# Kernel optimization log

Hardware: AMD Instinct MI355X
Metric: run time of the kernel (lower is better)

Reference implementation:

```python
import jax, jax.numpy as jnp
from jax import lax
import numpy as np

B, S, HID = 1, 1024, 4096
H, D = 64, 64  # num_heads, head_size (hidden = H*D)


def setup_inputs() -> dict:
    key = jax.random.key(0)
    ks = jax.random.split(key, 14)
    s = 0.02  # weight init scale
    return {
        "hidden": jax.random.normal(ks[0], (B, S, HID), jnp.float32),
        "w_key": jax.random.normal(ks[1], (HID, HID), jnp.float32) * s,
        "w_value": jax.random.normal(ks[2], (HID, HID), jnp.float32) * s,
        "w_receptance": jax.random.normal(ks[3], (HID, HID), jnp.float32) * s,
        "w_gate": jax.random.normal(ks[4], (HID, HID), jnp.float32) * s,
        "w_output": jax.random.normal(ks[5], (HID, HID), jnp.float32) * s,
        "time_mix_key": jax.random.uniform(ks[6], (HID,), jnp.float32),
        "time_mix_value": jax.random.uniform(ks[7], (HID,), jnp.float32),
        "time_mix_receptance": jax.random.uniform(ks[8], (HID,), jnp.float32),
        "time_mix_gate": jax.random.uniform(ks[9], (HID,), jnp.float32),
        "time_decay": jax.random.normal(ks[10], (H, D), jnp.float32) * 0.5,
        "time_faaaa": jax.random.normal(ks[11], (H, D), jnp.float32) * 0.5,
        "gn_weight": jnp.ones((HID,), jnp.float32),
        "gn_bias": jnp.zeros((HID,), jnp.float32),
    }


def reference(hidden, w_key, w_value, w_receptance, w_gate, w_output,
              time_mix_key, time_mix_value, time_mix_receptance, time_mix_gate,
              time_decay, time_faaaa, gn_weight, gn_bias):
    b, s, hid = hidden.shape
    h, d = time_decay.shape

    # time_shift: shifted[t] = hidden[t-1], shifted[0] = 0 (state is None)
    shifted = jnp.concatenate([jnp.zeros_like(hidden[:, :1]), hidden[:, :-1]], axis=1)

    def mix(m):
        return hidden * m + shifted * (1.0 - m)

    k = mix(time_mix_key) @ w_key.T            # (b, s, hid)
    v = mix(time_mix_value) @ w_value.T
    r = mix(time_mix_receptance) @ w_receptance.T
    g = jax.nn.silu(mix(time_mix_gate) @ w_gate.T)

    def heads(x):  # (b, s, hid) -> (s, b, h, d) for scan over time
        return x.reshape(b, s, h, d).transpose(1, 0, 2, 3)

    kh, vh, rh = heads(k), heads(v), heads(r)

    td = jnp.exp(-jnp.exp(time_decay))[None, :, :, None]  # (1, h, d, 1)
    tf = time_faaaa[None, :, :, None]                      # (1, h, d, 1)

    def step(state, rkv):
        r_t, k_t, v_t = rkv                                # each (b, h, d)
        a = k_t[..., :, None] * v_t[..., None, :]          # (b, h, d, d) outer product
        o = jnp.einsum('bhd,bhde->bhe', r_t, tf * a + state)
        return a + td * state, o

    state0 = jnp.zeros((b, h, d, d), jnp.float32)
    _, out = lax.scan(step, state0, (rh, kh, vh))          # out: (s, b, h, d)
    out = out.transpose(1, 0, 2, 3).reshape(b, s, hid)

    # GroupNorm(num_groups=h, channels=hid) over flattened tokens
    x = out.reshape(b * s, h, d)
    mu = x.mean(-1, keepdims=True)
    var = x.var(-1, keepdims=True)
    xn = (x - mu) * lax.rsqrt(var + 1e-5)
    xn = xn.reshape(b * s, hid) * gn_weight + gn_bias
    xn = xn.reshape(b, s, hid)

    return (g * xn) @ w_output.T
```

## Files before the change

kernel.cpp:

```cpp
#include <hip/hip_runtime.h>

#define S_LEN 1024
#define HIDN  4096
#define NH    64
#define HD    64
#define NCH   32
#define CLEN  32

typedef short bf16x8 __attribute__((ext_vector_type(8)));
typedef float f32x4  __attribute__((ext_vector_type(4)));

__device__ __forceinline__ unsigned short f2bf(float x){
  unsigned u = __float_as_uint(x);
  u += 0x7fffu + ((u >> 16) & 1u);
  return (unsigned short)(u >> 16);
}

__device__ __forceinline__ void gload_lds16(const void* g, void* l){
  __builtin_amdgcn_global_load_lds(
      (const __attribute__((address_space(1))) void*)g,
      (__attribute__((address_space(3))) void*)l, 16, 0, 0);
}

__global__ __launch_bounds__(256)
void wconv_kernel(const float* __restrict__ w0, const float* __restrict__ w1,
                  const float* __restrict__ w2, const float* __restrict__ w3,
                  const float* __restrict__ w4, unsigned short* __restrict__ out)
{
  const int z = blockIdx.y;
  const float* __restrict__ w = (z==0)?w0:(z==1)?w1:(z==2)?w2:(z==3)?w3:w4;
  const size_t idx = (size_t)blockIdx.x * 2048 + (size_t)threadIdx.x * 8;
  float4 a = *(const float4*)(w + idx);
  float4 b = *(const float4*)(w + idx + 4);
  ushort4 lo, hi;
  lo.x = f2bf(a.x); lo.y = f2bf(a.y); lo.z = f2bf(a.z); lo.w = f2bf(a.w);
  hi.x = f2bf(b.x); hi.y = f2bf(b.y); hi.z = f2bf(b.z); hi.w = f2bf(b.w);
  unsigned short* o = out + (size_t)z * HIDN * HIDN + idx;
  *(ushort4*)(o)     = lo;
  *(ushort4*)(o + 4) = hi;
}

__global__ __launch_bounds__(256)
void mix_kernel(const float* __restrict__ hidden,
                const float* __restrict__ tmk, const float* __restrict__ tmv,
                const float* __restrict__ tmr, const float* __restrict__ tmg,
                unsigned short* __restrict__ mixed)
{
  int idx = blockIdx.x * 256 + threadIdx.x;
  int i = idx & (HIDN - 1);
  float h  = hidden[idx];
  float sh = (idx >= HIDN) ? hidden[idx - HIDN] : 0.f;
  float mk = tmk[i], mv = tmv[i], mr = tmr[i], mg = tmg[i];
  mixed[idx + 0 * S_LEN * HIDN] = f2bf(h * mk + sh * (1.f - mk));
  mixed[idx + 1 * S_LEN * HIDN] = f2bf(h * mv + sh * (1.f - mv));
  mixed[idx + 2 * S_LEN * HIDN] = f2bf(h * mr + sh * (1.f - mr));
  mixed[idx + 3 * S_LEN * HIDN] = f2bf(h * mg + sh * (1.f - mg));
}

__global__ __launch_bounds__(256)
void gemm_lds(const unsigned short* __restrict__ Aall,
              const unsigned short* __restrict__ Wall,
              float* __restrict__ Call, int silu_mask, int nzper)
{
  const int bid  = blockIdx.x;
  const int xcd  = bid & 7;
  const int slot = bid >> 3;
  const int mt   = slot & 7;
  const int nz   = xcd * nzper + (slot >> 3);
  const int nt   = nz & 31;
  const int z    = nz >> 5;

  const unsigned short* __restrict__ A = Aall + (size_t)z * S_LEN * HIDN;
  const unsigned short* __restrict__ W = Wall + (size_t)z * HIDN * HIDN;
  float* __restrict__ C = Call + (size_t)z * S_LEN * HIDN;
  const int m0 = mt * 128;
  const int n0 = nt * 128;

  __shared__ unsigned short As[2][128 * 32];
  __shared__ unsigned short Bs[2][128 * 32];

  const int tid  = threadIdx.x;
  const int lane = tid & 63;
  const int wave = tid >> 6;
  const int wr = (wave >> 1) * 64;
  const int wc = (wave & 1) * 64;
  const int fr = lane & 15;
  const int fk = (lane >> 4) * 8;

  const int q0 = tid, q1 = 256 + tid;
  const int r0 = q0 >> 2, c0 = (q0 & 3) * 8;
  const int r1 = q1 >> 2, c1 = (q1 & 3) * 8;
  const unsigned short* A0 = A + (size_t)(m0 + r0) * HIDN + c0;
  const unsigned short* A1 = A + (size_t)(m0 + r1) * HIDN + c1;
  const unsigned short* W0 = W + (size_t)(n0 + r0) * HIDN + c0;
  const unsigned short* W1 = W + (size_t)(n0 + r1) * HIDN + c1;

  f32x4 acc[4][4];
#pragma unroll
  for (int mi = 0; mi < 4; ++mi)
#pragma unroll
    for (int ni = 0; ni < 4; ++ni) acc[mi][ni] = (f32x4){0.f, 0.f, 0.f, 0.f};

  for (int k0 = 0; k0 < HIDN; k0 += 64) {
    gload_lds16(A0 + k0,      &As[0][q0 * 8]);
    gload_lds16(A1 + k0,      &As[0][q1 * 8]);
    gload_lds16(A0 + k0 + 32, &As[1][q0 * 8]);
    gload_lds16(A1 + k0 + 32, &As[1][q1 * 8]);
    gload_lds16(W0 + k0,      &Bs[0][q0 * 8]);
    gload_lds16(W1 + k0,      &Bs[0][q1 * 8]);
    gload_lds16(W0 + k0 + 32, &Bs[1][q0 * 8]);
    gload_lds16(W1 + k0 + 32, &Bs[1][q1 * 8]);
    __syncthreads();

#pragma unroll
    for (int kk = 0; kk < 2; ++kk) {
      bf16x8 af[4], bq[4];
#pragma unroll
      for (int mi = 0; mi < 4; ++mi)
        af[mi] = *(const bf16x8*)(&As[kk][(wr + mi * 16 + fr) * 32 + fk]);
#pragma unroll
      for (int ni = 0; ni < 4; ++ni)
        bq[ni] = *(const bf16x8*)(&Bs[kk][(wc + ni * 16 + fr) * 32 + fk]);
#pragma unroll
      for (int mi = 0; mi < 4; ++mi)
#pragma unroll
        for (int ni = 0; ni < 4; ++ni)
          acc[mi][ni] = __builtin_amdgcn_mfma_f32_16x16x32_bf16(af[mi], bq[ni], acc[mi][ni], 0, 0, 0);
    }
    __syncthreads();
  }

  const bool do_silu = (silu_mask >> z) & 1;
  const int orow = (lane >> 4) * 4;
#pragma unroll
  for (int mi = 0; mi < 4; ++mi)
#pragma unroll
    for (int ni = 0; ni < 4; ++ni)
#pragma unroll
      for (int r = 0; r < 4; ++r) {
        int row = m0 + wr + mi * 16 + orow + r;
        int col = n0 + wc + ni * 16 + fr;
        float v = acc[mi][ni][r];
        if (do_silu) v = v / (1.f + __expf(-v));
        C[(size_t)row * HIDN + col] = v;
      }
}

__global__ __launch_bounds__(256)
void gemm_splitk(const unsigned short* __restrict__ A,
                 const unsigned short* __restrict__ W,
                 float* __restrict__ C)
{
  const int bid  = blockIdx.x;
  const int xcd  = bid & 7;
  const int slot = bid >> 3;
  const int mt   = slot & 7;
  const int nl   = (slot >> 3) & 3;
  const int ks   = slot >> 5;
  const int nt   = xcd * 4 + nl;
  const int m0 = mt * 128, n0 = nt * 128;
  const int kb = ks * (HIDN / 2), ke = kb + (HIDN / 2);

  __shared__ unsigned short As[2][128 * 32];
  __shared__ unsigned short Bs[2][128 * 32];

  const int tid  = threadIdx.x;
  const int lane = tid & 63;
  const int wave = tid >> 6;
  const int wr = (wave >> 1) * 64;
  const int wc = (wave & 1) * 64;
  const int fr = lane & 15;
  const int fk = (lane >> 4) * 8;

  const int q0 = tid, q1 = 256 + tid;
  const int r0 = q0 >> 2, c0 = (q0 & 3) * 8;
  const int r1 = q1 >> 2, c1 = (q1 & 3) * 8;
  const unsigned short* A0 = A + (size_t)(m0 + r0) * HIDN + c0;
  const unsigned short* A1 = A + (size_t)(m0 + r1) * HIDN + c1;
  const unsigned short* W0 = W + (size_t)(n0 + r0) * HIDN + c0;
  const unsigned short* W1 = W + (size_t)(n0 + r1) * HIDN + c1;

  f32x4 acc[4][4];
#pragma unroll
  for (int mi = 0; mi < 4; ++mi)
#pragma unroll
    for (int ni = 0; ni < 4; ++ni) acc[mi][ni] = (f32x4){0.f, 0.f, 0.f, 0.f};

  for (int k0 = kb; k0 < ke; k0 += 64) {
    gload_lds16(A0 + k0,      &As[0][q0 * 8]);
    gload_lds16(A1 + k0,      &As[0][q1 * 8]);
    gload_lds16(A0 + k0 + 32, &As[1][q0 * 8]);
    gload_lds16(A1 + k0 + 32, &As[1][q1 * 8]);
    gload_lds16(W0 + k0,      &Bs[0][q0 * 8]);
    gload_lds16(W1 + k0,      &Bs[0][q1 * 8]);
    gload_lds16(W0 + k0 + 32, &Bs[1][q0 * 8]);
    gload_lds16(W1 + k0 + 32, &Bs[1][q1 * 8]);
    __syncthreads();

#pragma unroll
    for (int kk = 0; kk < 2; ++kk) {
      bf16x8 af[4], bq[4];
#pragma unroll
      for (int mi = 0; mi < 4; ++mi)
        af[mi] = *(const bf16x8*)(&As[kk][(wr + mi * 16 + fr) * 32 + fk]);
#pragma unroll
      for (int ni = 0; ni < 4; ++ni)
        bq[ni] = *(const bf16x8*)(&Bs[kk][(wc + ni * 16 + fr) * 32 + fk]);
#pragma unroll
      for (int mi = 0; mi < 4; ++mi)
#pragma unroll
        for (int ni = 0; ni < 4; ++ni)
          acc[mi][ni] = __builtin_amdgcn_mfma_f32_16x16x32_bf16(af[mi], bq[ni], acc[mi][ni], 0, 0, 0);
    }
    __syncthreads();
  }

  const int orow = (lane >> 4) * 4;
#pragma unroll
  for (int mi = 0; mi < 4; ++mi)
#pragma unroll
    for (int ni = 0; ni < 4; ++ni)
#pragma unroll
      for (int r = 0; r < 4; ++r) {
        int row = m0 + wr + mi * 16 + orow + r;
        int col = n0 + wc + ni * 16 + fr;
        atomicAdd(&C[(size_t)row * HIDN + col], acc[mi][ni][r]);
      }
}

__global__ __launch_bounds__(64)
void rec_pass1(const float* __restrict__ kb, const float* __restrict__ vb,
               const float* __restrict__ time_decay, float* __restrict__ X)
{
  const int c = blockIdx.x, h = blockIdx.y, e = threadIdx.x;
  const float tde = __expf(-__expf(time_decay[h * 64 + e]));
  float td[64];
#pragma unroll
  for (int d = 0; d < 64; ++d) td[d] = __shfl(tde, d, 64);
  float st[64];
#pragma unroll
  for (int d = 0; d < 64; ++d) st[d] = 0.f;

  for (int t = c * CLEN; t < c * CLEN + CLEN; ++t) {
    const size_t off = (size_t)t * HIDN + h * 64;
    const float vl = vb[off + e];
    const float* __restrict__ krow = kb + off;
#pragma unroll
    for (int d = 0; d < 64; ++d)
      st[d] = fmaf(td[d], st[d], krow[d] * vl);
  }
#pragma unroll
  for (int d = 0; d < 64; ++d)
    X[(((size_t)c * NH + h) * 64 + d) * 64 + e] = st[d];
}

__global__ __launch_bounds__(64)
void rec_pass2(const float* __restrict__ time_decay,
               const float* __restrict__ X, float* __restrict__ Y)
{
  const int h = blockIdx.x, dq = blockIdx.y, e = threadIdx.x;
  float tdc[16];
#pragma unroll
  for (int i = 0; i < 16; ++i)
    tdc[i] = __expf(-(float)CLEN * __expf(time_decay[h * 64 + dq * 16 + i]));
  float acc[16];
#pragma unroll
  for (int i = 0; i < 16; ++i) acc[i] = 0.f;
  for (int c = 0; c < NCH; ++c) {
#pragma unroll
    for (int i = 0; i < 16; ++i) {
      size_t idx = (((size_t)c * NH + h) * 64 + dq * 16 + i) * 64 + e;
      Y[idx] = acc[i];
      acc[i] = fmaf(tdc[i], acc[i], X[idx]);
    }
  }
}

__global__ __launch_bounds__(64)
void rec_pass3(const float* __restrict__ kb, const float* __restrict__ vb,
               const float* __restrict__ rb, const float* __restrict__ gb,
               const float* __restrict__ time_decay, const float* __restrict__ time_faaaa,
               const float* __restrict__ gnw, const float* __restrict__ gnb,
               const float* __restrict__ Y, unsigned short* __restrict__ A2)
{
  const int c = blockIdx.x, h = blockIdx.y, e = threadIdx.x;
  const float tde = __expf(-__expf(time_decay[h * 64 + e]));
  float td[64];
#pragma unroll
  for (int d = 0; d < 64; ++d) td[d] = __shfl(tde, d, 64);
  float st[64];
#pragma unroll
  for (int d = 0; d < 64; ++d)
    st[d] = Y[(((size_t)c * NH + h) * 64 + d) * 64 + e];

  const float tf_l  = time_faaaa[h * 64 + e];
  const float gnw_l = gnw[h * 64 + e];
  const float gnb_l = gnb[h * 64 + e];

  for (int t = c * CLEN; t < c * CLEN + CLEN; ++t) {
    const size_t off = (size_t)t * HIDN + h * 64;
    const float kl = kb[off + e], rl = rb[off + e];
    const float vl = vb[off + e], gl = gb[off + e];

    float Asum = rl * tf_l * kl;
#pragma unroll
    for (int i = 1; i < 64; i <<= 1) Asum += __shfl_xor(Asum, i, 64);

    const float* __restrict__ krow = kb + off;
    const float* __restrict__ rrow = rb + off;
    float dot = 0.f;
#pragma unroll
    for (int d = 0; d < 64; ++d) {
      dot   = fmaf(rrow[d], st[d], dot);
      st[d] = fmaf(td[d], st[d], krow[d] * vl);
    }
    float o = fmaf(Asum, vl, dot);

    float s1 = o, s2 = o * o;
#pragma unroll
    for (int i = 1; i < 64; i <<= 1) {
      s1 += __shfl_xor(s1, i, 64);
      s2 += __shfl_xor(s2, i, 64);
    }
    float mean = s1 * (1.f / 64.f);
    float var  = s2 * (1.f / 64.f) - mean * mean;
    float xn   = (o - mean) * rsqrtf(var + 1e-5f);
    float yv   = xn * gnw_l + gnb_l;
    A2[off + e] = f2bf(gl * yv);
  }
}

extern "C" void kernel_launch(void* const* d_in, const int* in_sizes, int n_in,
                              void* d_out, int out_size, void* d_ws, size_t ws_size,
                              hipStream_t stream)
{
  const float* hidden     = (const float*)d_in[0];
  const float* w_key      = (const float*)d_in[1];
  const float* w_value    = (const float*)d_in[2];
  const float* w_recep    = (const float*)d_in[3];
  const float* w_gate     = (const float*)d_in[4];
  const float* w_output   = (const float*)d_in[5];
  const float* tmk        = (const float*)d_in[6];
  const float* tmv        = (const float*)d_in[7];
  const float* tmr        = (const float*)d_in[8];
  const float* tmg        = (const float*)d_in[9];
  const float* time_decay = (const float*)d_in[10];
  const float* time_faaaa = (const float*)d_in[11];
  const float* gnw        = (const float*)d_in[12];
  const float* gnb        = (const float*)d_in[13];
  float* out = (float*)d_out;

  char* ws = (char*)d_ws;
  unsigned short* wbf   = (unsigned short*)(ws);
  float*          Y     = (float*)(ws);
  unsigned short* mixed = (unsigned short*)(ws + 167772160);
  float*          X     = (float*)(ws + 167772160);
  float*          kvrg  = (float*)(ws + 201326592);
  unsigned short* A2    = (unsigned short*)(ws + 268435456);

  const float* kb = kvrg + 0 * (size_t)S_LEN * HIDN;
  const float* vb = kvrg + 1 * (size_t)S_LEN * HIDN;
  const float* rb = kvrg + 2 * (size_t)S_LEN * HIDN;
  const float* gb = kvrg + 3 * (size_t)S_LEN * HIDN;

  wconv_kernel<<<dim3(HIDN * HIDN / 2048, 5), 256, 0, stream>>>(
      w_key, w_value, w_recep, w_gate, w_output, wbf);

  mix_kernel<<<dim3(S_LEN * HIDN / 256), 256, 0, stream>>>(hidden, tmk, tmv, tmr, tmg, mixed);

  gemm_lds<<<dim3(1024), 256, 0, stream>>>(mixed, wbf, kvrg, 0x8, 16);

  rec_pass1<<<dim3(NCH, NH), 64, 0, stream>>>(kb, vb, time_decay, X);
  rec_pass2<<<dim3(NH, 4), 64, 0, stream>>>(time_decay, X, Y);
  rec_pass3<<<dim3(NCH, NH), 64, 0, stream>>>(kb, vb, rb, gb, time_decay, time_faaaa,
                                              gnw, gnb, Y, A2);

  hipMemsetAsync(d_out, 0, (size_t)out_size * sizeof(float), stream);
  gemm_splitk<<<dim3(512), 256, 0, stream>>>(A2, wbf + 4 * (size_t)HIDN * HIDN, out);
}
```

Measured before the change: 709.2 us.

## Replace split-K output GEMM with 64x128 tiles and spread pass2 over more blocks

The output projection no longer uses split-K with atomic adds into a zeroed buffer. It now uses 64x128 tiles over the full K range with plain stores, which also removes the memset. The grid stays at 512 blocks. Separately, rec_pass2 uses 16 d-groups of 4 instead of 4 groups of 16, giving more blocks for the sequential chunk scan. The trade-off is that smaller M tiles mean more redundant weight-tile loads and lower MFMA work per LDS load in the GEMM.

After: 710.1 us. About the same (+0.1%).

```diff
diff --git a/kernel.cpp b/kernel.cpp
--- a/kernel.cpp
+++ b/kernel.cpp
@@ -147,50 +147,46 @@
 }
 
 __global__ __launch_bounds__(256)
-void gemm_splitk(const unsigned short* __restrict__ A,
-                 const unsigned short* __restrict__ W,
-                 float* __restrict__ C)
+void gemm_out(const unsigned short* __restrict__ A,
+              const unsigned short* __restrict__ W,
+              float* __restrict__ C)
 {
   const int bid  = blockIdx.x;
   const int xcd  = bid & 7;
   const int slot = bid >> 3;
-  const int mt   = slot & 7;
-  const int nl   = (slot >> 3) & 3;
-  const int ks   = slot >> 5;
+  const int mt   = slot & 15;
+  const int nl   = slot >> 4;
   const int nt   = xcd * 4 + nl;
-  const int m0 = mt * 128, n0 = nt * 128;
-  const int kb = ks * (HIDN / 2), ke = kb + (HIDN / 2);
-
-  __shared__ unsigned short As[2][128 * 32];
+  const int m0 = mt * 64, n0 = nt * 128;
+
+  __shared__ unsigned short As[2][64 * 32];
   __shared__ unsigned short Bs[2][128 * 32];
 
   const int tid  = threadIdx.x;
   const int lane = tid & 63;
   const int wave = tid >> 6;
-  const int wr = (wave >> 1) * 64;
+  const int wr = (wave >> 1) * 32;
   const int wc = (wave & 1) * 64;
   const int fr = lane & 15;
   const int fk = (lane >> 4) * 8;
 
+  const int ra = tid >> 2, ca = (tid & 3) * 8;
   const int q0 = tid, q1 = 256 + tid;
-  const int r0 = q0 >> 2, c0 = (q0 & 3) * 8;
-  const int r1 = q1 >> 2, c1 = (q1 & 3) * 8;
-  const unsigned short* A0 = A + (size_t)(m0 + r0) * HIDN + c0;
-  const unsigned short* A1 = A + (size_t)(m0 + r1) * HIDN + c1;
-  const unsigned short* W0 = W + (size_t)(n0 + r0) * HIDN + c0;
-  const unsigned short* W1 = W + (size_t)(n0 + r1) * HIDN + c1;
-
-  f32x4 acc[4][4];
-#pragma unroll
-  for (int mi = 0; mi < 4; ++mi)
+  const int rb0 = q0 >> 2, cb0 = (q0 & 3) * 8;
+  const int rb1 = q1 >> 2, cb1 = (q1 & 3) * 8;
+  const unsigned short* Ap = A + (size_t)(m0 + ra) * HIDN + ca;
+  const unsigned short* W0 = W + (size_t)(n0 + rb0) * HIDN + cb0;
+  const unsigned short* W1 = W + (size_t)(n0 + rb1) * HIDN + cb1;
+
+  f32x4 acc[2][4];
+#pragma unroll
+  for (int mi = 0; mi < 2; ++mi)
 #pragma unroll
     for (int ni = 0; ni < 4; ++ni) acc[mi][ni] = (f32x4){0.f, 0.f, 0.f, 0.f};
 
-  for (int k0 = kb; k0 < ke; k0 += 64) {
-    gload_lds16(A0 + k0,      &As[0][q0 * 8]);
-    gload_lds16(A1 + k0,      &As[0][q1 * 8]);
-    gload_lds16(A0 + k0 + 32, &As[1][q0 * 8]);
-    gload_lds16(A1 + k0 + 32, &As[1][q1 * 8]);
+  for (int k0 = 0; k0 < HIDN; k0 += 64) {
+    gload_lds16(Ap + k0,      &As[0][tid * 8]);
+    gload_lds16(Ap + k0 + 32, &As[1][tid * 8]);
     gload_lds16(W0 + k0,      &Bs[0][q0 * 8]);
     gload_lds16(W1 + k0,      &Bs[0][q1 * 8]);
     gload_lds16(W0 + k0 + 32, &Bs[1][q0 * 8]);
@@ -199,15 +195,15 @@
 
 #pragma unroll
     for (int kk = 0; kk < 2; ++kk) {
-      bf16x8 af[4], bq[4];
-#pragma unroll
-      for (int mi = 0; mi < 4; ++mi)
+      bf16x8 af[2], bq[4];
+#pragma unroll
+      for (int mi = 0; mi < 2; ++mi)
         af[mi] = *(const bf16x8*)(&As[kk][(wr + mi * 16 + fr) * 32 + fk]);
 #pragma unroll
       for (int ni = 0; ni < 4; ++ni)
         bq[ni] = *(const bf16x8*)(&Bs[kk][(wc + ni * 16 + fr) * 32 + fk]);
 #pragma unroll
-      for (int mi = 0; mi < 4; ++mi)
+      for (int mi = 0; mi < 2; ++mi)
 #pragma unroll
         for (int ni = 0; ni < 4; ++ni)
           acc[mi][ni] = __builtin_amdgcn_mfma_f32_16x16x32_bf16(af[mi], bq[ni], acc[mi][ni], 0, 0, 0);
@@ -217,14 +213,14 @@
 
   const int orow = (lane >> 4) * 4;
 #pragma unroll
-  for (int mi = 0; mi < 4; ++mi)
+  for (int mi = 0; mi < 2; ++mi)
 #pragma unroll
     for (int ni = 0; ni < 4; ++ni)
 #pragma unroll
       for (int r = 0; r < 4; ++r) {
         int row = m0 + wr + mi * 16 + orow + r;
         int col = n0 + wc + ni * 16 + fr;
-        atomicAdd(&C[(size_t)row * HIDN + col], acc[mi][ni][r]);
+        C[(size_t)row * HIDN + col] = acc[mi][ni][r];
       }
 }
 
@@ -259,17 +255,17 @@
                const float* __restrict__ X, float* __restrict__ Y)
 {
   const int h = blockIdx.x, dq = blockIdx.y, e = threadIdx.x;
-  float tdc[16];
-#pragma unroll
-  for (int i = 0; i < 16; ++i)
-    tdc[i] = __expf(-(float)CLEN * __expf(time_decay[h * 64 + dq * 16 + i]));
-  float acc[16];
-#pragma unroll
-  for (int i = 0; i < 16; ++i) acc[i] = 0.f;
+  float tdc[4];
+#pragma unroll
+  for (int i = 0; i < 4; ++i)
+    tdc[i] = __expf(-(float)CLEN * __expf(time_decay[h * 64 + dq * 4 + i]));
+  float acc[4];
+#pragma unroll
+  for (int i = 0; i < 4; ++i) acc[i] = 0.f;
   for (int c = 0; c < NCH; ++c) {
 #pragma unroll
-    for (int i = 0; i < 16; ++i) {
-      size_t idx = (((size_t)c * NH + h) * 64 + dq * 16 + i) * 64 + e;
+    for (int i = 0; i < 4; ++i) {
+      size_t idx = (((size_t)c * NH + h) * 64 + dq * 4 + i) * 64 + e;
       Y[idx] = acc[i];
       acc[i] = fmaf(tdc[i], acc[i], X[idx]);
     }
@@ -371,10 +367,9 @@
   gemm_lds<<<dim3(1024), 256, 0, stream>>>(mixed, wbf, kvrg, 0x8, 16);
 
   rec_pass1<<<dim3(NCH, NH), 64, 0, stream>>>(kb, vb, time_decay, X);
-  rec_pass2<<<dim3(NH, 4), 64, 0, stream>>>(time_decay, X, Y);
+  rec_pass2<<<dim3(NH, 16), 64, 0, stream>>>(time_decay, X, Y);
   rec_pass3<<<dim3(NCH, NH), 64, 0, stream>>>(kb, vb, rb, gb, time_decay, time_faaaa,
                                               gnw, gnb, Y, A2);
 
-  hipMemsetAsync(d_out, 0, (size_t)out_size * sizeof(float), stream);
-  gemm_splitk<<<dim3(512), 256, 0, stream>>>(A2, wbf + 4 * (size_t)HIDN * HIDN, out);
-}
+  gemm_out<<<dim3(512), 256, 0, stream>>>(A2, wbf + 4 * (size_t)HIDN * HIDN, out);
+}
```
